# Performance work log

Measured on AMD Instinct MI355X. Metric: run time of the kernel, lower is better.

The kernel has to match this reference:

```python
import jax, jax.numpy as jnp
import numpy as np

K_TOP = 2  # top-k experts per token


def setup_inputs() -> dict:
    key = jax.random.key(0)
    k1, k2, k3 = jax.random.split(key, 3)
    B, S, H, E = 4, 2048, 1024, 8
    hidden_states = jax.random.normal(k1, (B, S, H), dtype=jnp.float32)
    router_w = jax.random.normal(k2, (E, H), dtype=jnp.float32) * 0.02
    expert_weights = jax.random.normal(k3, (E, H, H), dtype=jnp.float32) * 0.02
    return {"hidden_states": hidden_states, "router_w": router_w, "expert_weights": expert_weights}


def reference(hidden_states, router_w, expert_weights):
    B, S, H = hidden_states.shape
    x = hidden_states.reshape(-1, H)                      # [N, H], N = B*S
    logits = x @ router_w.T                               # [N, E]
    probs = jax.nn.softmax(logits, axis=-1)               # [N, E]
    topk_vals, topk_idx = jax.lax.top_k(probs, K_TOP)     # [N, K]
    topk_w = topk_vals / (topk_vals.sum(-1, keepdims=True) + 1e-6)  # [N, K]

    # Dense per-expert GEMM over all tokens (single-device dispatch = identity)
    expert_out = jnp.einsum('nh,eho->eno', x, expert_weights)  # [E, N, H]

    # all_to_all_combine: gather each token's K expert outputs
    combined = jnp.take_along_axis(
        expert_out.transpose(1, 0, 2),                    # [N, E, H]
        topk_idx[:, :, None], axis=1)                     # [N, K, H]
    combined = combined.transpose(1, 0, 2)                # [K, N, H]

    # remap bias: sum over last dim of one-hot(topk_idx) * router_prob == gathered prob
    remap_bias = jnp.take_along_axis(probs, topk_idx, axis=1).T[:, :, None]  # [K, N, 1]

    weights = topk_w.T[:, :, None]                        # [K, N, 1]
    out = ((combined + remap_bias) * weights).sum(axis=0) # [N, H]
    return out.reshape(B, S, H)
```

## Files before the change

kernel.cpp:

```cpp
#include <hip/hip_runtime.h>
#include <hip/hip_fp16.h>
#include <cstdint>

typedef unsigned short u16;
typedef __attribute__((ext_vector_type(8))) short short8;
typedef __attribute__((ext_vector_type(4))) float float4v;

#define NTOK 8192
#define HDIM 1024
#define NEXP 8
#define TM 128
#define TN 128
#define BK 64
#define MAXT 136

__device__ __forceinline__ u16 f2bf(float f) {
    union { float f; uint32_t u; } v; v.f = f;
    uint32_t u = v.u;
    return (u16)((u + 0x7FFFu + ((u >> 16) & 1u)) >> 16);
}

__device__ __forceinline__ void gll16(const u16* g, u16* l) {
    __builtin_amdgcn_global_load_lds(
        (const __attribute__((address_space(1))) uint32_t*)g,
        (__attribute__((address_space(3))) uint32_t*)l,
        16, 0, 0);
}

__global__ __launch_bounds__(256) void prep_w(const float* __restrict__ w,
                                              u16* __restrict__ wt) {
    __shared__ float tile[32][33];
    const int e  = blockIdx.z;
    const int k0 = blockIdx.x * 32;
    const int n0 = blockIdx.y * 32;
    const int r = threadIdx.x >> 3;
    const int c = (threadIdx.x & 7) * 4;
    const float4 v = *(const float4*)(w + ((size_t)e << 20) + (size_t)(k0 + r) * HDIM + n0 + c);
    tile[r][c] = v.x; tile[r][c+1] = v.y; tile[r][c+2] = v.z; tile[r][c+3] = v.w;
    __syncthreads();
    ushort4 o;
    o.x = f2bf(tile[c][r]); o.y = f2bf(tile[c+1][r]);
    o.z = f2bf(tile[c+2][r]); o.w = f2bf(tile[c+3][r]);
    *(ushort4*)(wt + ((size_t)e << 20) + (size_t)(n0 + r) * HDIM + k0 + c) = o;
}

__global__ __launch_bounds__(256) void router(const float* __restrict__ x,
                                              const float* __restrict__ rw,
                                              u16* __restrict__ x_bf,
                                              float* __restrict__ wt0,
                                              float* __restrict__ wt1,
                                              float* __restrict__ biasv,
                                              int* __restrict__ sel) {
    const int wv = threadIdx.x >> 6;
    const int l  = threadIdx.x & 63;
    const int n  = blockIdx.x * 4 + wv;
    const float4* xr = (const float4*)(x + (size_t)n * HDIM);
    ushort4* xo = (ushort4*)(x_bf + (size_t)n * HDIM);

    float4 xv[4];
#pragma unroll
    for (int t = 0; t < 4; t++) {
        xv[t] = xr[t * 64 + l];
        ushort4 p;
        p.x = f2bf(xv[t].x); p.y = f2bf(xv[t].y);
        p.z = f2bf(xv[t].z); p.w = f2bf(xv[t].w);
        xo[t * 64 + l] = p;
    }

    float logits[NEXP];
#pragma unroll
    for (int e = 0; e < NEXP; e++) {
        const float4* rwe = (const float4*)(rw + e * HDIM);
        float acc = 0.f;
#pragma unroll
        for (int t = 0; t < 4; t++) {
            const float4 r = rwe[t * 64 + l];
            acc += xv[t].x * r.x + xv[t].y * r.y + xv[t].z * r.z + xv[t].w * r.w;
        }
#pragma unroll
        for (int s = 32; s > 0; s >>= 1) acc += __shfl_xor(acc, s, 64);
        logits[e] = acc;
    }

    if (l == 0) {
        float mx = logits[0];
#pragma unroll
        for (int e = 1; e < NEXP; e++) mx = fmaxf(mx, logits[e]);
        float p[NEXP]; float sum = 0.f;
#pragma unroll
        for (int e = 0; e < NEXP; e++) { p[e] = expf(logits[e] - mx); sum += p[e]; }
        const float inv = 1.f / sum;
#pragma unroll
        for (int e = 0; e < NEXP; e++) p[e] *= inv;
        int e0 = 0;
#pragma unroll
        for (int e = 1; e < NEXP; e++) if (p[e] > p[e0]) e0 = e;
        int e1 = (e0 == 0) ? 1 : 0;
#pragma unroll
        for (int e = 0; e < NEXP; e++) if (e != e0 && p[e] > p[e1]) e1 = e;
        const float p0 = p[e0], p1 = p[e1];
        const float wsum = p0 + p1 + 1e-6f;
        const float w0 = p0 / wsum, w1 = p1 / wsum;
        wt0[n] = w0; wt1[n] = w1;
        biasv[n] = w0 * p0 + w1 * p1;
        sel[n] = e0 | (e1 << 8);
    }
}

__global__ __launch_bounds__(256) void build_lists(const int* __restrict__ sel,
                                                   int* __restrict__ lists,
                                                   int* __restrict__ counts) {
    const int n  = blockIdx.x * 256 + threadIdx.x;
    const int wv = threadIdx.x >> 6;
    const int l  = threadIdx.x & 63;
    const int s  = sel[n];
    const int e0 = s & 0xFF, e1 = s >> 8;
    __shared__ int wcnt[NEXP][4];
    __shared__ int ebase[NEXP];
    int pf0 = 0, pf1 = 0;
    const unsigned long long ltmask = (1ULL << l) - 1ULL;
#pragma unroll
    for (int e = 0; e < NEXP; e++) {
        const int slot = (e0 == e) ? 0 : ((e1 == e) ? 1 : -1);
        const unsigned long long bal = __ballot(slot >= 0);
        const int pf = __popcll(bal & ltmask);
        if (slot == 0) pf0 = pf;
        if (slot == 1) pf1 = pf;
        if (l == 0) wcnt[e][wv] = __popcll(bal);
    }
    __syncthreads();
    if (threadIdx.x < NEXP) {
        const int e = threadIdx.x;
        const int tot = wcnt[e][0] + wcnt[e][1] + wcnt[e][2] + wcnt[e][3];
        ebase[e] = atomicAdd(&counts[e * 16], tot);
    }
    __syncthreads();
    int off0 = ebase[e0], off1 = ebase[e1];
#pragma unroll
    for (int i = 0; i < 4; i++) {
        off0 += (i < wv) ? wcnt[e0][i] : 0;
        off1 += (i < wv) ? wcnt[e1][i] : 0;
    }
    lists[e0 * NTOK + off0 + pf0] = n;
    lists[e1 * NTOK + off1 + pf1] = n | 0x10000;
}

__global__ __launch_bounds__(64) void plan_tiles(const int* __restrict__ counts,
                                                 int* __restrict__ tmap) {
    if (threadIdx.x == 0) {
        int idx = 0;
        for (int e = 0; e < NEXP; e++) {
            const int nt = (counts[e * 16] + TM - 1) / TM;
            for (int m = 0; m < nt; m++) tmap[idx++] = (e << 16) | m;
        }
        for (int i = idx; i < MAXT; i++) tmap[i] = -1;
    }
}

__global__ __launch_bounds__(256) void moe_gemm(const u16* __restrict__ x_bf,
                                                const u16* __restrict__ wt_bf,
                                                const int* __restrict__ lists,
                                                const int* __restrict__ counts,
                                                const int* __restrict__ tmap,
                                                const float* __restrict__ wt0,
                                                const float* __restrict__ wt1,
                                                const float* __restrict__ biasv,
                                                __half* __restrict__ stage0,
                                                __half* __restrict__ stage1) {
    const int ent = tmap[blockIdx.x];
    if (ent < 0) return;
    const int e = ent >> 16;
    const int tile_m = (ent & 0xFFFF) * TM;
    const int cnt = counts[e * 16];
    const int tn = blockIdx.y * TN;

    __shared__ u16 lA[TM * BK];
    __shared__ u16 lB[TN * BK];
    __shared__ int   toks[TM];
    __shared__ float wgt[TM];
    __shared__ float bia[TM];
    __shared__ int   slt[TM];

    const int t  = threadIdx.x;
    const int wv = t >> 6;
    const int l  = t & 63;

    if (t < TM) {
        const int idx = tile_m + t;
        int tok = 0; float w = 0.f, b = 0.f; int sl = 0;
        if (idx < cnt) {
            const int entry = lists[e * NTOK + idx];
            tok = entry & 0xFFFF;
            sl = entry >> 16;
            w = sl ? wt1[tok] : wt0[tok];
            b = sl ? 0.f : biasv[tok];
        }
        toks[t] = tok; wgt[t] = w; bia[t] = b; slt[t] = sl;
    }
    __syncthreads();

    const int r_in = l >> 3;
    const int koff = (((l & 7) ^ r_in)) * 8;
    const u16* pA[4]; const u16* pB[4]; u16* qA[4]; u16* qB[4];
#pragma unroll
    for (int i = 0; i < 4; i++) {
        const int c = wv * 4 + i;
        const int row = c * 8 + r_in;
        pA[i] = x_bf + (size_t)toks[row] * HDIM + koff;
        pB[i] = wt_bf + ((size_t)e << 20) + (size_t)(tn + row) * HDIM + koff;
        qA[i] = lA + c * 512;
        qB[i] = lB + c * 512;
    }

    const int wm = (wv & 1) * 64;
    const int wn = (wv >> 1) * 64;
    const int fm = l & 15;
    const int fq = l >> 4;
    int aoff[4], boff[4];
#pragma unroll
    for (int i = 0; i < 4; i++) {
        const int ra = wm + i * 16 + fm;
        const int rb = wn + i * 16 + fm;
        aoff[i] = ra * 64 + ((fq ^ (ra & 7)) * 8);
        boff[i] = rb * 64 + ((fq ^ (rb & 7)) * 8);
    }

    float4v acc[4][4];
#pragma unroll
    for (int i = 0; i < 4; i++)
#pragma unroll
        for (int j = 0; j < 4; j++) { float4v z = {0.f, 0.f, 0.f, 0.f}; acc[i][j] = z; }

    for (int k0 = 0; k0 < HDIM; k0 += BK) {
        __syncthreads();
#pragma unroll
        for (int i = 0; i < 4; i++) {
            gll16(pA[i] + k0, qA[i]);
            gll16(pB[i] + k0, qB[i]);
        }
        __syncthreads();

#pragma unroll
        for (int kh = 0; kh < 2; kh++) {
            short8 af[4], bf[4];
#pragma unroll
            for (int mf = 0; mf < 4; mf++)
                af[mf] = *(const short8*)&lA[aoff[mf] ^ (kh << 5)];
#pragma unroll
            for (int nf = 0; nf < 4; nf++)
                bf[nf] = *(const short8*)&lB[boff[nf] ^ (kh << 5)];
#pragma unroll
            for (int mf = 0; mf < 4; mf++)
#pragma unroll
                for (int nf = 0; nf < 4; nf++)
                    acc[mf][nf] = __builtin_amdgcn_mfma_f32_16x16x32_bf16(af[mf], bf[nf], acc[mf][nf], 0, 0, 0);
        }
    }

#pragma unroll
    for (int mf = 0; mf < 4; mf++) {
#pragma unroll
        for (int r = 0; r < 4; r++) {
            const int m_local = wm + mf * 16 + fq * 4 + r;
            if (tile_m + m_local < cnt) {
                const int tok = toks[m_local];
                const float w = wgt[m_local], b = bia[m_local];
                __half* sp = (slt[m_local] ? stage1 : stage0) + (size_t)tok * HDIM;
#pragma unroll
                for (int nf = 0; nf < 4; nf++) {
                    const int h = tn + wn + nf * 16 + fm;
                    sp[h] = __float2half(acc[mf][nf][r] * w + b);
                }
            }
        }
    }
}

__global__ __launch_bounds__(256) void combine(const __half* __restrict__ s0,
                                               const __half* __restrict__ s1,
                                               float* __restrict__ out) {
    const size_t idx = ((size_t)blockIdx.x * 256 + threadIdx.x) * 8;
    union { uint4 v; __half h[8]; } a, b;
    a.v = *(const uint4*)(s0 + idx);
    b.v = *(const uint4*)(s1 + idx);
    float4 o0, o1;
    o0.x = __half2float(a.h[0]) + __half2float(b.h[0]);
    o0.y = __half2float(a.h[1]) + __half2float(b.h[1]);
    o0.z = __half2float(a.h[2]) + __half2float(b.h[2]);
    o0.w = __half2float(a.h[3]) + __half2float(b.h[3]);
    o1.x = __half2float(a.h[4]) + __half2float(b.h[4]);
    o1.y = __half2float(a.h[5]) + __half2float(b.h[5]);
    o1.z = __half2float(a.h[6]) + __half2float(b.h[6]);
    o1.w = __half2float(a.h[7]) + __half2float(b.h[7]);
    *(float4*)(out + idx)     = o0;
    *(float4*)(out + idx + 4) = o1;
}

extern "C" void kernel_launch(void* const* d_in, const int* in_sizes, int n_in,
                              void* d_out, int out_size, void* d_ws, size_t ws_size,
                              hipStream_t stream) {
    const float* x  = (const float*)d_in[0];
    const float* rw = (const float*)d_in[1];
    const float* ew = (const float*)d_in[2];
    float* out = (float*)d_out;

    char* ws = (char*)d_ws;
    u16*    x_bf   = (u16*)ws;
    u16*    w_bf   = (u16*)(ws + 16777216);
    __half* stage0 = (__half*)(ws + 33554432);
    __half* stage1 = (__half*)(ws + 50331648);
    float*  wt0    = (float*)(ws + 67108864);
    float*  wt1    = (float*)(ws + 67141632);
    float*  biasv  = (float*)(ws + 67174400);
    int*    sel    = (int*)(ws + 67207168);
    int*    lists  = (int*)(ws + 67239936);
    int*    counts = (int*)(ws + 67502080);
    int*    tmap   = (int*)(ws + 67502592);

    hipMemsetAsync(counts, 0, NEXP * 16 * sizeof(int), stream);

    prep_w<<<dim3(32, 32, NEXP), 256, 0, stream>>>(ew, w_bf);
    router<<<NTOK / 4, 256, 0, stream>>>(x, rw, x_bf, wt0, wt1, biasv, sel);
    build_lists<<<NTOK / 256, 256, 0, stream>>>(sel, lists, counts);
    plan_tiles<<<1, 64, 0, stream>>>(counts, tmap);
    moe_gemm<<<dim3(MAXT, HDIM / TN, 1), 256, 0, stream>>>(
        x_bf, w_bf, lists, counts, tmap, wt0, wt1, biasv, stage0, stage1);
    combine<<<(NTOK * HDIM) / (256 * 8), 256, 0, stream>>>(stage0, stage1, out);
}
```

Before: 200.6 us.

## Merge prep kernels, fold tile planning into build_lists, drop memset

Merges the weight transpose/convert and router kernels into one launch and zeroes the counters inside it instead of using a separate memset. Tile planning moves into the last block of build_lists through an atomic completion counter, removing a single-thread kernel launch. The GEMM grid is transposed so consecutive blocks share the same expert/M tile across N tiles, which may improve L2 reuse of the activations. The trade-off is an extra threadfence and atomic in build_lists, plus a dependence on ctrl being zeroed before build_lists runs.

```diff
diff --git a/kernel.cpp b/kernel.cpp
--- a/kernel.cpp
+++ b/kernel.cpp
@@ -13,6 +13,8 @@
 #define TN 128
 #define BK 64
 #define MAXT 136
+#define WBLK 8192
+#define RBLK 2048
 
 __device__ __forceinline__ u16 f2bf(float f) {
     union { float f; uint32_t u; } v; v.f = f;
@@ -27,89 +29,95 @@
         16, 0, 0);
 }
 
-__global__ __launch_bounds__(256) void prep_w(const float* __restrict__ w,
-                                              u16* __restrict__ wt) {
-    __shared__ float tile[32][33];
-    const int e  = blockIdx.z;
-    const int k0 = blockIdx.x * 32;
-    const int n0 = blockIdx.y * 32;
-    const int r = threadIdx.x >> 3;
-    const int c = (threadIdx.x & 7) * 4;
-    const float4 v = *(const float4*)(w + ((size_t)e << 20) + (size_t)(k0 + r) * HDIM + n0 + c);
-    tile[r][c] = v.x; tile[r][c+1] = v.y; tile[r][c+2] = v.z; tile[r][c+3] = v.w;
-    __syncthreads();
-    ushort4 o;
-    o.x = f2bf(tile[c][r]); o.y = f2bf(tile[c+1][r]);
-    o.z = f2bf(tile[c+2][r]); o.w = f2bf(tile[c+3][r]);
-    *(ushort4*)(wt + ((size_t)e << 20) + (size_t)(n0 + r) * HDIM + k0 + c) = o;
-}
-
-__global__ __launch_bounds__(256) void router(const float* __restrict__ x,
-                                              const float* __restrict__ rw,
-                                              u16* __restrict__ x_bf,
-                                              float* __restrict__ wt0,
-                                              float* __restrict__ wt1,
-                                              float* __restrict__ biasv,
-                                              int* __restrict__ sel) {
-    const int wv = threadIdx.x >> 6;
-    const int l  = threadIdx.x & 63;
-    const int n  = blockIdx.x * 4 + wv;
-    const float4* xr = (const float4*)(x + (size_t)n * HDIM);
-    ushort4* xo = (ushort4*)(x_bf + (size_t)n * HDIM);
-
-    float4 xv[4];
-#pragma unroll
-    for (int t = 0; t < 4; t++) {
-        xv[t] = xr[t * 64 + l];
-        ushort4 p;
-        p.x = f2bf(xv[t].x); p.y = f2bf(xv[t].y);
-        p.z = f2bf(xv[t].z); p.w = f2bf(xv[t].w);
-        xo[t * 64 + l] = p;
-    }
-
-    float logits[NEXP];
-#pragma unroll
-    for (int e = 0; e < NEXP; e++) {
-        const float4* rwe = (const float4*)(rw + e * HDIM);
-        float acc = 0.f;
+__global__ __launch_bounds__(256) void prep(const float* __restrict__ x,
+                                            const float* __restrict__ rw,
+                                            const float* __restrict__ ew,
+                                            u16* __restrict__ x_bf,
+                                            u16* __restrict__ w_bf,
+                                            float* __restrict__ wt0,
+                                            float* __restrict__ wt1,
+                                            float* __restrict__ biasv,
+                                            int* __restrict__ sel,
+                                            int* __restrict__ ctrl) {
+    if (blockIdx.x == 0 && threadIdx.x < 132) ctrl[threadIdx.x] = 0;
+
+    if (blockIdx.x < WBLK) {
+        __shared__ float tile[32][33];
+        const int bid = blockIdx.x;
+        const int e  = bid >> 10;
+        const int k0 = (bid & 31) * 32;
+        const int n0 = ((bid >> 5) & 31) * 32;
+        const int r = threadIdx.x >> 3;
+        const int c = (threadIdx.x & 7) * 4;
+        const float4 v = *(const float4*)(ew + ((size_t)e << 20) + (size_t)(k0 + r) * HDIM + n0 + c);
+        tile[r][c] = v.x; tile[r][c+1] = v.y; tile[r][c+2] = v.z; tile[r][c+3] = v.w;
+        __syncthreads();
+        ushort4 o;
+        o.x = f2bf(tile[c][r]); o.y = f2bf(tile[c+1][r]);
+        o.z = f2bf(tile[c+2][r]); o.w = f2bf(tile[c+3][r]);
+        *(ushort4*)(w_bf + ((size_t)e << 20) + (size_t)(n0 + r) * HDIM + k0 + c) = o;
+    } else {
+        const int wv = threadIdx.x >> 6;
+        const int l  = threadIdx.x & 63;
+        const int n  = (blockIdx.x - WBLK) * 4 + wv;
+        const float4* xr = (const float4*)(x + (size_t)n * HDIM);
+        ushort4* xo = (ushort4*)(x_bf + (size_t)n * HDIM);
+
+        float4 xv[4];
 #pragma unroll
         for (int t = 0; t < 4; t++) {
-            const float4 r = rwe[t * 64 + l];
-            acc += xv[t].x * r.x + xv[t].y * r.y + xv[t].z * r.z + xv[t].w * r.w;
-        }
-#pragma unroll
-        for (int s = 32; s > 0; s >>= 1) acc += __shfl_xor(acc, s, 64);
-        logits[e] = acc;
-    }
-
-    if (l == 0) {
-        float mx = logits[0];
-#pragma unroll
-        for (int e = 1; e < NEXP; e++) mx = fmaxf(mx, logits[e]);
-        float p[NEXP]; float sum = 0.f;
-#pragma unroll
-        for (int e = 0; e < NEXP; e++) { p[e] = expf(logits[e] - mx); sum += p[e]; }
-        const float inv = 1.f / sum;
-#pragma unroll
-        for (int e = 0; e < NEXP; e++) p[e] *= inv;
-        int e0 = 0;
-#pragma unroll
-        for (int e = 1; e < NEXP; e++) if (p[e] > p[e0]) e0 = e;
-        int e1 = (e0 == 0) ? 1 : 0;
-#pragma unroll
-        for (int e = 0; e < NEXP; e++) if (e != e0 && p[e] > p[e1]) e1 = e;
-        const float p0 = p[e0], p1 = p[e1];
-        const float wsum = p0 + p1 + 1e-6f;
-        const float w0 = p0 / wsum, w1 = p1 / wsum;
-        wt0[n] = w0; wt1[n] = w1;
-        biasv[n] = w0 * p0 + w1 * p1;
-        sel[n] = e0 | (e1 << 8);
+            xv[t] = xr[t * 64 + l];
+            ushort4 p;
+            p.x = f2bf(xv[t].x); p.y = f2bf(xv[t].y);
+            p.z = f2bf(xv[t].z); p.w = f2bf(xv[t].w);
+            xo[t * 64 + l] = p;
+        }
+
+        float logits[NEXP];
+#pragma unroll
+        for (int e = 0; e < NEXP; e++) {
+            const float4* rwe = (const float4*)(rw + e * HDIM);
+            float acc = 0.f;
+#pragma unroll
+            for (int t = 0; t < 4; t++) {
+                const float4 r = rwe[t * 64 + l];
+                acc += xv[t].x * r.x + xv[t].y * r.y + xv[t].z * r.z + xv[t].w * r.w;
+            }
+#pragma unroll
+            for (int s = 32; s > 0; s >>= 1) acc += __shfl_xor(acc, s, 64);
+            logits[e] = acc;
+        }
+
+        if (l == 0) {
+            float mx = logits[0];
+#pragma unroll
+            for (int e = 1; e < NEXP; e++) mx = fmaxf(mx, logits[e]);
+            float p[NEXP]; float sum = 0.f;
+#pragma unroll
+            for (int e = 0; e < NEXP; e++) { p[e] = expf(logits[e] - mx); sum += p[e]; }
+            const float inv = 1.f / sum;
+#pragma unroll
+            for (int e = 0; e < NEXP; e++) p[e] *= inv;
+            int e0 = 0;
+#pragma unroll
+            for (int e = 1; e < NEXP; e++) if (p[e] > p[e0]) e0 = e;
+            int e1 = (e0 == 0) ? 1 : 0;
+#pragma unroll
+            for (int e = 0; e < NEXP; e++) if (e != e0 && p[e] > p[e1]) e1 = e;
+            const float p0 = p[e0], p1 = p[e1];
+            const float wsum = p0 + p1 + 1e-6f;
+            const float w0 = p0 / wsum, w1 = p1 / wsum;
+            wt0[n] = w0; wt1[n] = w1;
+            biasv[n] = w0 * p0 + w1 * p1;
+            sel[n] = e0 | (e1 << 8);
+        }
     }
 }
 
 __global__ __launch_bounds__(256) void build_lists(const int* __restrict__ sel,
                                                    int* __restrict__ lists,
-                                                   int* __restrict__ counts) {
+                                                   int* __restrict__ ctrl,
+                                                   int* __restrict__ tmap) {
     const int n  = blockIdx.x * 256 + threadIdx.x;
     const int wv = threadIdx.x >> 6;
     const int l  = threadIdx.x & 63;
@@ -132,7 +140,7 @@
     if (threadIdx.x < NEXP) {
         const int e = threadIdx.x;
         const int tot = wcnt[e][0] + wcnt[e][1] + wcnt[e][2] + wcnt[e][3];
-        ebase[e] = atomicAdd(&counts[e * 16], tot);
+        ebase[e] = atomicAdd(&ctrl[e * 16], tot);
     }
     __syncthreads();
     int off0 = ebase[e0], off1 = ebase[e1];
@@ -143,36 +151,48 @@
     }
     lists[e0 * NTOK + off0 + pf0] = n;
     lists[e1 * NTOK + off1 + pf1] = n | 0x10000;
-}
-
-__global__ __launch_bounds__(64) void plan_tiles(const int* __restrict__ counts,
-                                                 int* __restrict__ tmap) {
-    if (threadIdx.x == 0) {
-        int idx = 0;
-        for (int e = 0; e < NEXP; e++) {
-            const int nt = (counts[e * 16] + TM - 1) / TM;
-            for (int m = 0; m < nt; m++) tmap[idx++] = (e << 16) | m;
-        }
-        for (int i = idx; i < MAXT; i++) tmap[i] = -1;
+
+    __shared__ int lastflag;
+    __threadfence();
+    if (threadIdx.x == 0) lastflag = (atomicAdd(&ctrl[128], 1) == (int)gridDim.x - 1);
+    __syncthreads();
+    if (lastflag) {
+        __shared__ int tbase[NEXP + 1];
+        if (threadIdx.x == 0) {
+            int acc = 0;
+            for (int e = 0; e < NEXP; e++) {
+                tbase[e] = acc;
+                acc += (atomicAdd(&ctrl[e * 16], 0) + TM - 1) / TM;
+            }
+            tbase[NEXP] = acc;
+        }
+        __syncthreads();
+        for (int i = threadIdx.x; i < MAXT; i += 256) {
+            int v = -1;
+#pragma unroll
+            for (int e = 0; e < NEXP; e++)
+                if (i >= tbase[e] && i < tbase[e + 1]) v = (e << 16) | (i - tbase[e]);
+            tmap[i] = v;
+        }
     }
 }
 
 __global__ __launch_bounds__(256) void moe_gemm(const u16* __restrict__ x_bf,
                                                 const u16* __restrict__ wt_bf,
                                                 const int* __restrict__ lists,
-                                                const int* __restrict__ counts,
+                                                const int* __restrict__ ctrl,
                                                 const int* __restrict__ tmap,
                                                 const float* __restrict__ wt0,
                                                 const float* __restrict__ wt1,
                                                 const float* __restrict__ biasv,
                                                 __half* __restrict__ stage0,
                                                 __half* __restrict__ stage1) {
-    const int ent = tmap[blockIdx.x];
+    const int ent = tmap[blockIdx.y];
     if (ent < 0) return;
     const int e = ent >> 16;
     const int tile_m = (ent & 0xFFFF) * TM;
-    const int cnt = counts[e * 16];
-    const int tn = blockIdx.y * TN;
+    const int cnt = ctrl[e * 16];
+    const int tn = blockIdx.x * TN;
 
     __shared__ u16 lA[TM * BK];
     __shared__ u16 lB[TN * BK];
@@ -314,16 +334,12 @@
     float*  biasv  = (float*)(ws + 67174400);
     int*    sel    = (int*)(ws + 67207168);
     int*    lists  = (int*)(ws + 67239936);
-    int*    counts = (int*)(ws + 67502080);
-    int*    tmap   = (int*)(ws + 67502592);
-
-    hipMemsetAsync(counts, 0, NEXP * 16 * sizeof(int), stream);
-
-    prep_w<<<dim3(32, 32, NEXP), 256, 0, stream>>>(ew, w_bf);
-    router<<<NTOK / 4, 256, 0, stream>>>(x, rw, x_bf, wt0, wt1, biasv, sel);
-    build_lists<<<NTOK / 256, 256, 0, stream>>>(sel, lists, counts);
-    plan_tiles<<<1, 64, 0, stream>>>(counts, tmap);
-    moe_gemm<<<dim3(MAXT, HDIM / TN, 1), 256, 0, stream>>>(
-        x_bf, w_bf, lists, counts, tmap, wt0, wt1, biasv, stage0, stage1);
+    int*    ctrl   = (int*)(ws + 67502080);
+    int*    tmap   = (int*)(ws + 67502720);
+
+    prep<<<WBLK + RBLK, 256, 0, stream>>>(x, rw, ew, x_bf, w_bf, wt0, wt1, biasv, sel, ctrl);
+    build_lists<<<NTOK / 256, 256, 0, stream>>>(sel, lists, ctrl, tmap);
+    moe_gemm<<<dim3(HDIM / TN, MAXT, 1), 256, 0, stream>>>(
+        x_bf, w_bf, lists, ctrl, tmap, wt0, wt1, biasv, stage0, stage1);
     combine<<<(NTOK * HDIM) / (256 * 8), 256, 0, stream>>>(stage0, stage1, out);
 }
```

Result: no change. 201.6 us (+0.5%).
